# Performance work log

Hardware: AMD Instinct MI355X
Metric: run time of the kernel (lower is better)

The kernel has to match this reference:

```python
import jax, jax.numpy as jnp
import numpy as np

NUM_HEADS = 12

def _get_rel_pos(size, rel_pos):
    # q_size == k_size == size, no interpolation needed (table has 2*size-1 rows)
    idx = jnp.arange(size)[:, None] - jnp.arange(size)[None, :] + (size - 1)  # (size,size)
    return rel_pos[idx]  # (size, size, head_dim)

def setup_inputs() -> dict:
    key = jax.random.key(0)
    ks = jax.random.split(key, 7)
    B, H, W, dim = 8, 32, 32, 768
    head_dim = dim // NUM_HEADS
    return {
        "x": jax.random.normal(ks[0], (B, H, W, dim), jnp.float32),
        "qkv_w": jax.random.normal(ks[1], (dim, 3 * dim), jnp.float32) * 0.02,
        "qkv_b": jax.random.normal(ks[2], (3 * dim,), jnp.float32) * 0.02,
        "proj_w": jax.random.normal(ks[3], (dim, dim), jnp.float32) * 0.02,
        "proj_b": jax.random.normal(ks[4], (dim,), jnp.float32) * 0.02,
        "rel_pos_h": jax.random.normal(ks[5], (2 * H - 1, head_dim), jnp.float32) * 0.02,
        "rel_pos_w": jax.random.normal(ks[6], (2 * W - 1, head_dim), jnp.float32) * 0.02,
    }

def reference(x, qkv_w, qkv_b, proj_w, proj_b, rel_pos_h, rel_pos_w):
    B, H, W, dim = x.shape
    N = H * W
    head_dim = dim // NUM_HEADS
    scale = head_dim ** (-0.5)

    qkv = x.reshape(B, N, dim) @ qkv_w + qkv_b                     # (B,N,3*dim)
    qkv = qkv.reshape(B, N, 3, NUM_HEADS, head_dim)
    qkv = qkv.transpose(2, 0, 3, 1, 4).reshape(3, B * NUM_HEADS, N, head_dim)
    q, k, v = qkv[0], qkv[1], qkv[2]                               # (B*h, N, hd)

    attn = jnp.einsum("bnd,bmd->bnm", q * scale, k)                # (B*h, N, N)

    # decomposed relative position bias
    Rh = _get_rel_pos(H, rel_pos_h)                                # (H,H,hd)
    Rw = _get_rel_pos(W, rel_pos_w)                                # (W,W,hd)
    r_q = q.reshape(B * NUM_HEADS, H, W, head_dim)
    rel_h = jnp.einsum("bhwc,hkc->bhwk", r_q, Rh)                  # (B*h,H,W,H)
    rel_w = jnp.einsum("bhwc,wkc->bhwk", r_q, Rw)                  # (B*h,H,W,W)
    attn = (attn.reshape(B * NUM_HEADS, H, W, H, W)
            + rel_h[:, :, :, :, None]
            + rel_w[:, :, :, None, :]).reshape(B * NUM_HEADS, N, N)

    attn = jax.nn.softmax(attn, axis=-1)
    out = jnp.einsum("bnm,bmd->bnd", attn, v)                      # (B*h, N, hd)
    out = out.reshape(B, NUM_HEADS, H, W, head_dim).transpose(0, 2, 3, 1, 4).reshape(B, H, W, dim)
    return out @ proj_w + proj_b
```

## Files before the change

kernel.cpp:

```cpp
#include <hip/hip_runtime.h>
#include <hip/hip_bf16.h>
#include <math.h>

#define DIM   768
#define NHEAD 12
#define NQ    1024

typedef short  short8  __attribute__((ext_vector_type(8)));
typedef unsigned short us8 __attribute__((ext_vector_type(8)));
typedef float  f32x16  __attribute__((ext_vector_type(16)));

#if __has_builtin(__builtin_amdgcn_exp2f)
#define EXP2(x) __builtin_amdgcn_exp2f(x)
#else
#define EXP2(x) __expf(0.69314718056f * (x))
#endif
#define LOG2E 1.44269504089f

__device__ inline ushort f2b(float f) {
  union { float f; unsigned u; } c; c.f = f;
  unsigned r = (c.u + 0x7FFFu + ((c.u >> 16) & 1u)) >> 16;
  return (ushort)r;
}
__device__ inline float b2f(ushort h) {
  union { unsigned u; float f; } c; c.u = ((unsigned)h) << 16;
  return c.f;
}
__device__ inline ushort4 cvt4(float4 v) {
  ushort4 o; o.x = f2b(v.x); o.y = f2b(v.y); o.z = f2b(v.z); o.w = f2b(v.w);
  return o;
}
__device__ inline unsigned pkr(float a, float b) {
  union { float f; unsigned u; } ca, cb; ca.f = a; cb.f = b;
  return __builtin_amdgcn_perm(cb.u + 0x8000u, ca.u + 0x8000u, 0x07060302u);
}
__device__ __forceinline__ void gload16(const void* g, void* l) {
  __builtin_amdgcn_global_load_lds(
      (const __attribute__((address_space(1))) void*)g,
      (__attribute__((address_space(3))) void*)l, 16, 0, 0);
}

__global__ __launch_bounds__(256) void prep(
    const float* __restrict__ x, const float* __restrict__ qkv_w,
    const float* __restrict__ proj_w, ushort* __restrict__ Xb,
    ushort* __restrict__ Wqt, ushort* __restrict__ Wpt) {
  __shared__ ushort Ts[64][68];
  const int blk = blockIdx.x, tid = threadIdx.x;
  if (blk < 768) {
    const float4* src = (const float4*)x;
    ushort4* dst = (ushort4*)Xb;
    int base = blk * 2048;
#pragma unroll
    for (int it = 0; it < 8; ++it) {
      int i = base + it * 256 + tid;
      dst[i] = cvt4(src[i]);
    }
    return;
  }
  const float* W; ushort* Wt; int ncols, tk, tn;
  if (blk < 1200) { int t = blk - 768;  W = qkv_w; Wt = Wqt; ncols = 2304; tk = t % 12; tn = t / 12; }
  else            { int t = blk - 1200; W = proj_w; Wt = Wpt; ncols = 768; tk = t % 12; tn = t / 12; }
  const int kb = tk * 64, nb = tn * 64;
#pragma unroll
  for (int rr = 0; rr < 4; ++rr) {
    int r = (tid >> 4) + rr * 16, c4 = (tid & 15) * 4;
    float4 w = *(const float4*)(W + (size_t)(kb + r) * ncols + nb + c4);
    *(ushort4*)&Ts[r][c4] = cvt4(w);
  }
  __syncthreads();
#pragma unroll
  for (int wwi = 0; wwi < 2; ++wwi) {
    int n = (tid >> 3) + wwi * 32, k8 = (tid & 7) * 8;
    us8 v;
#pragma unroll
    for (int j = 0; j < 8; ++j) v[j] = Ts[k8 + j][n];
    *(us8*)(Wt + (size_t)(nb + n) * 768 + kb + k8) = v;
  }
}

__global__ __launch_bounds__(256, 4) void gemm_qkv(
    const ushort* __restrict__ A, const ushort* __restrict__ BT,
    const float* __restrict__ bias, ushort* __restrict__ Cp,
    ushort* __restrict__ VTg) {
  __shared__ __align__(16) ushort As[128 * 64];
  __shared__ __align__(16) ushort Bs[128 * 64];
  const int tid = threadIdx.x;
  const int flat = blockIdx.x;
  const int g = flat >> 3;
  const int by = (flat & 7) * 8 + g / 18;
  const int bx = g % 18;
  const int bm = by * 128, bn = bx * 128;
  const int lane = tid & 63, wv = tid >> 6;
  const int l31 = lane & 31, lh = lane >> 5;
  const int wm = (wv >> 1) * 64, wn = (wv & 1) * 64;
  const int xr = l31 & 7;

  const int dr = lane >> 3;
  const int ccol = ((lane & 7) ^ dr) * 8;
  const ushort* ag = A + (size_t)(bm + wv * 32 + dr) * 768 + ccol;
  const ushort* bg = BT + (size_t)(bn + wv * 32 + dr) * 768 + ccol;
  ushort* al = &As[wv * 32 * 64];
  ushort* bl = &Bs[wv * 32 * 64];

  f32x16 acc[2][2];
#pragma unroll
  for (int i = 0; i < 2; ++i)
#pragma unroll
    for (int j = 0; j < 2; ++j)
#pragma unroll
      for (int r = 0; r < 16; ++r) acc[i][j][r] = 0.f;

  for (int kt = 0; kt < 768; kt += 64) {
    __syncthreads();
#pragma unroll
    for (int wi = 0; wi < 4; ++wi) {
      gload16(ag + kt + wi * (8 * 768), al + wi * 512);
      gload16(bg + kt + wi * (8 * 768), bl + wi * 512);
    }
    __syncthreads();
#pragma unroll
    for (int ks = 0; ks < 4; ++ks) {
      const int ca = ((ks * 2 + lh) ^ xr) * 8;
      short8 a0 = *(const short8*)&As[(wm + l31) * 64 + ca];
      short8 a1 = *(const short8*)&As[(wm + 32 + l31) * 64 + ca];
      short8 b0 = *(const short8*)&Bs[(wn + l31) * 64 + ca];
      short8 b1 = *(const short8*)&Bs[(wn + 32 + l31) * 64 + ca];
      acc[0][0] = __builtin_amdgcn_mfma_f32_32x32x16_bf16(a0, b0, acc[0][0], 0, 0, 0);
      acc[0][1] = __builtin_amdgcn_mfma_f32_32x32x16_bf16(a0, b1, acc[0][1], 0, 0, 0);
      acc[1][0] = __builtin_amdgcn_mfma_f32_32x32x16_bf16(a1, b0, acc[1][0], 0, 0, 0);
      acc[1][1] = __builtin_amdgcn_mfma_f32_32x32x16_bf16(a1, b1, acc[1][1], 0, 0, 0);
    }
  }

  if (bn < 1536) {
#pragma unroll
    for (int mb = 0; mb < 2; ++mb)
#pragma unroll
      for (int nb = 0; nb < 2; ++nb) {
        int col = bn + wn + nb * 32 + l31;
        float bv = bias[col];
#pragma unroll
        for (int reg = 0; reg < 16; ++reg) {
          int row = bm + wm + mb * 32 + (reg & 3) + 8 * (reg >> 2) + 4 * lh;
          Cp[(size_t)row * 2304 + col] = f2b(acc[mb][nb][reg] + bv);
        }
      }
  } else {
    const int b_ = bm >> 10;
    const int nbase = (bm & 1023) + wm;
#pragma unroll
    for (int nb = 0; nb < 2; ++nb) {
      int col = bn + wn + nb * 32 + l31;
      float bv = bias[col];
      int hd_ = col - 1536;
      int h_ = hd_ >> 6, d_ = hd_ & 63;
      ushort* vrow = VTg + ((size_t)(b_ * NHEAD + h_) * 64 + d_) * NQ;
#pragma unroll
      for (int mb = 0; mb < 2; ++mb)
#pragma unroll
        for (int g2 = 0; g2 < 4; ++g2) {
          int n = nbase + mb * 32 + 8 * g2 + 4 * lh;
          ushort4 st;
          st.x = f2b(acc[mb][nb][4 * g2 + 0] + bv);
          st.y = f2b(acc[mb][nb][4 * g2 + 1] + bv);
          st.z = f2b(acc[mb][nb][4 * g2 + 2] + bv);
          st.w = f2b(acc[mb][nb][4 * g2 + 3] + bv);
          *(ushort4*)(vrow + n) = st;
        }
    }
  }
}

__global__ __launch_bounds__(256, 4) void gemm_proj(
    const ushort* __restrict__ A, const ushort* __restrict__ BT,
    const float* __restrict__ bias, float* __restrict__ C) {
  __shared__ __align__(16) ushort As[128 * 64];
  __shared__ __align__(16) ushort Bs[64 * 64];
  const int tid = threadIdx.x;
  const int flat = blockIdx.x;
  const int g = flat >> 3;
  const int by = (flat & 7) * 8 + g / 12;
  const int bx = g % 12;
  const int bm = by * 128, bn = bx * 64;
  const int lane = tid & 63, wv = tid >> 6;
  const int l31 = lane & 31, lh = lane >> 5;
  const int wm = (wv >> 1) * 64, wn = (wv & 1) * 32;
  const int xr = l31 & 7;

  const int dr = lane >> 3;
  const int ccol = ((lane & 7) ^ dr) * 8;
  const ushort* ag = A + (size_t)(bm + wv * 32 + dr) * 768 + ccol;
  const ushort* bg = BT + (size_t)(bn + wv * 16 + dr) * 768 + ccol;
  ushort* al = &As[wv * 32 * 64];
  ushort* bl = &Bs[wv * 16 * 64];

  f32x16 acc0, acc1;
#pragma unroll
  for (int r = 0; r < 16; ++r) { acc0[r] = 0.f; acc1[r] = 0.f; }

  for (int kt = 0; kt < 768; kt += 64) {
    __syncthreads();
#pragma unroll
    for (int wi = 0; wi < 4; ++wi)
      gload16(ag + kt + wi * (8 * 768), al + wi * 512);
    gload16(bg + kt,            bl);
    gload16(bg + kt + 8 * 768,  bl + 512);
    __syncthreads();
#pragma unroll
    for (int ks = 0; ks < 4; ++ks) {
      const int ca = ((ks * 2 + lh) ^ xr) * 8;
      short8 a0 = *(const short8*)&As[(wm + l31) * 64 + ca];
      short8 a1 = *(const short8*)&As[(wm + 32 + l31) * 64 + ca];
      short8 b0 = *(const short8*)&Bs[(wn + l31) * 64 + ca];
      acc0 = __builtin_amdgcn_mfma_f32_32x32x16_bf16(a0, b0, acc0, 0, 0, 0);
      acc1 = __builtin_amdgcn_mfma_f32_32x32x16_bf16(a1, b0, acc1, 0, 0, 0);
    }
  }

  const int col = bn + wn + l31;
  const float bv = bias[col];
#pragma unroll
  for (int reg = 0; reg < 16; ++reg) {
    int row = bm + wm + (reg & 3) + 8 * (reg >> 2) + 4 * lh;
    C[(size_t)row * 768 + col]        = acc0[reg] + bv;
    C[(size_t)(row + 32) * 768 + col] = acc1[reg] + bv;
  }
}

__global__ __launch_bounds__(256, 4) void attn_mfma(
    const ushort* __restrict__ QKV, const ushort* __restrict__ VTg,
    const float* __restrict__ rph, const float* __restrict__ rpw,
    ushort* __restrict__ O) {
  __shared__ ushort Qs[128][72];
  __shared__ __align__(16) ushort KV[2 * 64 * 64];

  ushort* const Ksp = KV;
  ushort* const VTp = KV + 64 * 64;

  const int tid = threadIdx.x;
  const int bh = blockIdx.x % 96;
  const int qt = blockIdx.x / 96;
  const int b = bh / NHEAD, h = bh % NHEAD;
  const int n0 = qt * 128;
  const int lane = tid & 63, wv = tid >> 6;
  const int l31 = lane & 31, lh = lane >> 5;
  const int wb = wv * 32;
  const int xr = l31 & 7;

  const ushort* qb = QKV + (size_t)b * NQ * 2304 + h * 64;
  const ushort* kb = qb + DIM;
  const ushort* vtg = VTg + (size_t)bh * 64 * NQ;

#pragma unroll
  for (int it = 0; it < 4; ++it) {
    int item = tid + 256 * it;
    int r = item >> 3, c8 = (item & 7) * 8;
    *(us8*)&Qs[r][c8] = *(const us8*)(qb + (size_t)(n0 + r) * 2304 + c8);
  }
#pragma unroll
  for (int it = 0; it < 4; ++it) {
    int item = tid + 256 * it;
    int r = item >> 4, c4 = (item & 15) * 4;
    if (r < 63) {
      float4 vh = *(const float4*)(rph + r * 64 + c4);
      vh.x *= LOG2E; vh.y *= LOG2E; vh.z *= LOG2E; vh.w *= LOG2E;
      *(ushort4*)&Ksp[r * 64 + c4] = cvt4(vh);
      float4 vw = *(const float4*)(rpw + r * 64 + c4);
      vw.x *= LOG2E; vw.y *= LOG2E; vw.z *= LOG2E; vw.w *= LOG2E;
      *(ushort4*)&VTp[r * 64 + c4] = cvt4(vw);
    } else {
      ushort4 z = {0, 0, 0, 0};
      *(ushort4*)&Ksp[r * 64 + c4] = z;
      *(ushort4*)&VTp[r * 64 + c4] = z;
    }
  }

  const int dr = lane >> 3;
  const int ccol = ((lane & 7) ^ dr) * 8;
  const ushort* kg = kb + (size_t)(wv * 16 + dr) * 2304 + ccol;
  const ushort* vg = vtg + (size_t)(wv * 16 + dr) * NQ + ccol;
  ushort* kl = &Ksp[wv * 16 * 64];
  ushort* vl = &VTp[wv * 16 * 64];

  __syncthreads();

  short8 aq[4];
#pragma unroll
  for (int ks = 0; ks < 4; ++ks)
    aq[ks] = *(const short8*)&Qs[wb + l31][ks * 16 + lh * 8];

  __syncthreads();

  ushort* Pb2 = &Qs[0][0] + wv * (32 * 40);
  ushort* rhs = &Qs[0][0] + 5120;

  {
    const int hq31 = qt * 4 + wv + 31;
    f32x16 sh;
#pragma unroll
    for (int i = 0; i < 16; ++i) sh[i] = 0.f;
#pragma unroll
    for (int ks = 0; ks < 4; ++ks) {
      short8 at = *(const short8*)&Ksp[(hq31 - l31) * 64 + ks * 16 + lh * 8];
      sh = __builtin_amdgcn_mfma_f32_32x32x16_bf16(at, aq[ks], sh, 0, 0, 0);
    }
#pragma unroll
    for (int reg = 0; reg < 16; ++reg) {
      int hk = (reg & 3) + 8 * (reg >> 2) + 4 * lh;
      rhs[hk * 128 + wb + l31] = f2b(sh[reg]);
    }
  }

  float rwv[16];
  {
    short8 at[8];
#pragma unroll
    for (int ub = 0; ub < 2; ++ub)
#pragma unroll
      for (int ks = 0; ks < 4; ++ks)
        at[ub * 4 + ks] =
            *(const short8*)&VTp[(ub * 32 + l31) * 64 + ks * 16 + lh * 8];
    f32x16 su0, su1;
#pragma unroll
    for (int i = 0; i < 16; ++i) { su0[i] = 0.f; su1[i] = 0.f; }
#pragma unroll
    for (int ks = 0; ks < 4; ++ks) {
      su0 = __builtin_amdgcn_mfma_f32_32x32x16_bf16(at[ks],     aq[ks], su0, 0, 0, 0);
      su1 = __builtin_amdgcn_mfma_f32_32x32x16_bf16(at[4 + ks], aq[ks], su1, 0, 0, 0);
    }
    __syncthreads();
#pragma unroll
    for (int reg = 0; reg < 16; ++reg) {
      int rm = (reg & 3) + 8 * (reg >> 2) + 4 * lh;
      KV[rm * 128 + wb + l31]        = f2b(su0[reg]);
      KV[(32 + rm) * 128 + wb + l31] = f2b(su1[reg]);
    }
#pragma unroll
    for (int reg = 0; reg < 16; ++reg) {
      int rm = (reg & 3) + 8 * (reg >> 2) + 4 * lh;
      rwv[reg] = b2f(KV[(31 + l31 - rm) * 128 + wb + l31]);
    }
  }

  f32x16 oacc0, oacc1;
#pragma unroll
  for (int i = 0; i < 16; ++i) { oacc0[i] = 0.f; oacc1[i] = 0.f; }
  float lacc = 0.f;

  for (int t = 0; t < 16; ++t) {
    const int kt = t * 64;
    __syncthreads();
    gload16(kg + (size_t)kt * 2304,              kl);
    gload16(kg + (size_t)kt * 2304 + 8 * 2304,   kl + 512);
    gload16(vg + kt,                             vl);
    gload16(vg + kt + 8 * NQ,                    vl + 512);
    __syncthreads();

    const float rh0 = b2f(rhs[(2 * t) * 128 + wb + l31]);
    const float rh1 = b2f(rhs[(2 * t + 1) * 128 + wb + l31]);

#pragma unroll
    for (int cb = 0; cb < 2; ++cb) {
      f32x16 s;
#pragma unroll
      for (int i = 0; i < 16; ++i) s[i] = 0.f;
#pragma unroll
      for (int ks = 0; ks < 4; ++ks) {
        const int ck = ((ks * 2 + lh) ^ xr) * 8;
        short8 ak = *(const short8*)&Ksp[(cb * 32 + l31) * 64 + ck];
        s = __builtin_amdgcn_mfma_f32_32x32x16_bf16(ak, aq[ks], s, 0, 0, 0);
      }
      const float rhv = cb ? rh1 : rh0;
#pragma unroll
      for (int g = 0; g < 4; ++g) {
        float p0 = EXP2(fmaf(s[4 * g + 0], 0.18033688f, rwv[4 * g + 0] + rhv));
        float p1 = EXP2(fmaf(s[4 * g + 1], 0.18033688f, rwv[4 * g + 1] + rhv));
        float p2 = EXP2(fmaf(s[4 * g + 2], 0.18033688f, rwv[4 * g + 2] + rhv));
        float p3 = EXP2(fmaf(s[4 * g + 3], 0.18033688f, rwv[4 * g + 3] + rhv));
        lacc += (p0 + p1) + (p2 + p3);
        uint2 pk; pk.x = pkr(p0, p1); pk.y = pkr(p2, p3);
        *(uint2*)&Pb2[l31 * 40 + 8 * g + 4 * lh] = pk;
      }
#pragma unroll
      for (int ks = 0; ks < 2; ++ks) {
        const int cv = ((cb * 4 + ks * 2 + lh) ^ xr) * 8;
        short8 ap  = *(const short8*)&Pb2[l31 * 40 + ks * 16 + lh * 8];
        short8 bv0 = *(const short8*)&VTp[l31 * 64 + cv];
        short8 bv1 = *(const short8*)&VTp[(32 + l31) * 64 + cv];
        oacc0 = __builtin_amdgcn_mfma_f32_32x32x16_bf16(ap, bv0, oacc0, 0, 0, 0);
        oacc1 = __builtin_amdgcn_mfma_f32_32x32x16_bf16(ap, bv1, oacc1, 0, 0, 0);
      }
    }
  }

  lacc += __shfl_xor(lacc, 32);
  const float linv = 1.0f / lacc;
  ushort* ob = O + ((size_t)b * NQ + n0 + wb) * DIM + h * 64;
#pragma unroll
  for (int reg = 0; reg < 16; ++reg) {
    int row = (reg & 3) + 8 * (reg >> 2) + 4 * lh;
    float lq = __shfl(linv, row);
    ob[(size_t)row * DIM + l31]      = f2b(oacc0[reg] * lq);
    ob[(size_t)row * DIM + 32 + l31] = f2b(oacc1[reg] * lq);
  }
}

extern "C" void kernel_launch(void* const* d_in, const int* in_sizes, int n_in,
                              void* d_out, int out_size, void* d_ws, size_t ws_size,
                              hipStream_t stream) {
  const float* x      = (const float*)d_in[0];
  const float* qkv_w  = (const float*)d_in[1];
  const float* qkv_b  = (const float*)d_in[2];
  const float* proj_w = (const float*)d_in[3];
  const float* proj_b = (const float*)d_in[4];
  const float* rel_h  = (const float*)d_in[5];
  const float* rel_w  = (const float*)d_in[6];
  float* out = (float*)d_out;

  ushort* qkvb = (ushort*)d_ws;
  ushort* obuf = qkvb + (size_t)8192 * 2304;
  ushort* Xb   = obuf + (size_t)8192 * DIM;
  ushort* Wqt  = Xb + (size_t)8192 * DIM;
  ushort* Wpt  = Wqt + (size_t)2304 * DIM;
  ushort* VTg  = Wpt + (size_t)DIM * DIM;

  prep<<<dim3(1344), 256, 0, stream>>>(x, qkv_w, proj_w, Xb, Wqt, Wpt);

  gemm_qkv<<<dim3(1152), 256, 0, stream>>>(Xb, Wqt, qkv_b, qkvb, VTg);

  attn_mfma<<<dim3(96 * 8), 256, 0, stream>>>(qkvb, VTg, rel_h, rel_w, obuf);

  gemm_proj<<<dim3(768), 256, 0, stream>>>(obuf, Wpt, proj_b, out);
}
```

Measured before the change: 192.6 us.

## Shrink attention LDS footprint to 32KB and raise occupancy to five blocks

Replaces the padded Q tile and separate K/V buffers with a single 32KB LDS array split into two regions, loads Q with direct global-to-LDS swizzled copies, and swizzles the rel-pos tables. The three rel-pos MFMA groups are now computed together after one barrier, and the P staging buffer drops its padding from 40 to 32 columns. The aim is to fit more blocks per CU (launch bounds 4 to 5) by cutting LDS and to remove a barrier in the prologue. The tighter register budget may cause spills, and the unpadded P buffer may see more bank conflicts.

```diff
diff --git a/kernel.cpp b/kernel.cpp
--- a/kernel.cpp
+++ b/kernel.cpp
@@ -227,15 +227,13 @@
   }
 }
 
-__global__ __launch_bounds__(256, 4) void attn_mfma(
+__global__ __launch_bounds__(256, 5) void attn_mfma(
     const ushort* __restrict__ QKV, const ushort* __restrict__ VTg,
     const float* __restrict__ rph, const float* __restrict__ rpw,
     ushort* __restrict__ O) {
-  __shared__ ushort Qs[128][72];
-  __shared__ __align__(16) ushort KV[2 * 64 * 64];
-
-  ushort* const Ksp = KV;
-  ushort* const VTp = KV + 64 * 64;
+  __shared__ __align__(16) ushort L[16384];
+  ushort* const R0 = L;
+  ushort* const R1 = L + 8192;
 
   const int tid = threadIdx.x;
   const int bh = blockIdx.x % 96;
@@ -251,96 +249,87 @@
   const ushort* kb = qb + DIM;
   const ushort* vtg = VTg + (size_t)bh * 64 * NQ;
 
-#pragma unroll
-  for (int it = 0; it < 4; ++it) {
-    int item = tid + 256 * it;
-    int r = item >> 3, c8 = (item & 7) * 8;
-    *(us8*)&Qs[r][c8] = *(const us8*)(qb + (size_t)(n0 + r) * 2304 + c8);
+  const int dr = lane >> 3;
+  const int ccol = ((lane & 7) ^ dr) * 8;
+
+  {
+    const ushort* qg = qb + (size_t)(n0 + wv * 32 + dr) * 2304 + ccol;
+    ushort* ql = R0 + wv * 32 * 64;
+#pragma unroll
+    for (int wi = 0; wi < 4; ++wi)
+      gload16(qg + (size_t)wi * 8 * 2304, ql + wi * 512);
   }
 #pragma unroll
   for (int it = 0; it < 4; ++it) {
     int item = tid + 256 * it;
     int r = item >> 4, c4 = (item & 15) * 4;
+    int sw = r * 64 + (((c4 >> 3) ^ (r & 7)) << 3) + (c4 & 7);
     if (r < 63) {
       float4 vh = *(const float4*)(rph + r * 64 + c4);
       vh.x *= LOG2E; vh.y *= LOG2E; vh.z *= LOG2E; vh.w *= LOG2E;
-      *(ushort4*)&Ksp[r * 64 + c4] = cvt4(vh);
+      *(ushort4*)&R1[sw] = cvt4(vh);
       float4 vw = *(const float4*)(rpw + r * 64 + c4);
       vw.x *= LOG2E; vw.y *= LOG2E; vw.z *= LOG2E; vw.w *= LOG2E;
-      *(ushort4*)&VTp[r * 64 + c4] = cvt4(vw);
+      *(ushort4*)&R1[4096 + sw] = cvt4(vw);
     } else {
       ushort4 z = {0, 0, 0, 0};
-      *(ushort4*)&Ksp[r * 64 + c4] = z;
-      *(ushort4*)&VTp[r * 64 + c4] = z;
-    }
-  }
-
-  const int dr = lane >> 3;
-  const int ccol = ((lane & 7) ^ dr) * 8;
+      *(ushort4*)&R1[sw] = z;
+      *(ushort4*)&R1[4096 + sw] = z;
+    }
+  }
+  __syncthreads();
+
+  short8 aq[4];
+#pragma unroll
+  for (int ks = 0; ks < 4; ++ks)
+    aq[ks] = *(const short8*)&R0[(wb + l31) * 64 + ((ks * 2 + lh) ^ xr) * 8];
+
+  const int rA = qt * 4 + wv + 31 - l31;
+  short8 ah[4];
+#pragma unroll
+  for (int ks = 0; ks < 4; ++ks)
+    ah[ks] = *(const short8*)&R1[rA * 64 + ((ks * 2 + lh) ^ (rA & 7)) * 8];
+  short8 aw[8];
+#pragma unroll
+  for (int ub = 0; ub < 2; ++ub) {
+    const int rB = ub * 32 + l31;
+#pragma unroll
+    for (int ks = 0; ks < 4; ++ks)
+      aw[ub * 4 + ks] =
+          *(const short8*)&R1[4096 + rB * 64 + ((ks * 2 + lh) ^ (rB & 7)) * 8];
+  }
+  __syncthreads();
+
+  f32x16 sh, su0, su1;
+#pragma unroll
+  for (int i = 0; i < 16; ++i) { sh[i] = 0.f; su0[i] = 0.f; su1[i] = 0.f; }
+#pragma unroll
+  for (int ks = 0; ks < 4; ++ks) {
+    sh  = __builtin_amdgcn_mfma_f32_32x32x16_bf16(ah[ks],     aq[ks], sh,  0, 0, 0);
+    su0 = __builtin_amdgcn_mfma_f32_32x32x16_bf16(aw[ks],     aq[ks], su0, 0, 0, 0);
+    su1 = __builtin_amdgcn_mfma_f32_32x32x16_bf16(aw[4 + ks], aq[ks], su1, 0, 0, 0);
+  }
+
+  ushort* Pb2 = R0 + wv * 1024;
+  ushort* rhs = R0 + 4096;
+#pragma unroll
+  for (int reg = 0; reg < 16; ++reg) {
+    int rm = (reg & 3) + 8 * (reg >> 2) + 4 * lh;
+    rhs[rm * 128 + wb + l31] = f2b(sh[reg]);
+    R1[rm * 128 + wb + l31]        = f2b(su0[reg]);
+    R1[(32 + rm) * 128 + wb + l31] = f2b(su1[reg]);
+  }
+  float rwv[16];
+#pragma unroll
+  for (int reg = 0; reg < 16; ++reg) {
+    int rm = (reg & 3) + 8 * (reg >> 2) + 4 * lh;
+    rwv[reg] = b2f(R1[(31 + l31 - rm) * 128 + wb + l31]);
+  }
+
   const ushort* kg = kb + (size_t)(wv * 16 + dr) * 2304 + ccol;
   const ushort* vg = vtg + (size_t)(wv * 16 + dr) * NQ + ccol;
-  ushort* kl = &Ksp[wv * 16 * 64];
-  ushort* vl = &VTp[wv * 16 * 64];
-
-  __syncthreads();
-
-  short8 aq[4];
-#pragma unroll
-  for (int ks = 0; ks < 4; ++ks)
-    aq[ks] = *(const short8*)&Qs[wb + l31][ks * 16 + lh * 8];
-
-  __syncthreads();
-
-  ushort* Pb2 = &Qs[0][0] + wv * (32 * 40);
-  ushort* rhs = &Qs[0][0] + 5120;
-
-  {
-    const int hq31 = qt * 4 + wv + 31;
-    f32x16 sh;
-#pragma unroll
-    for (int i = 0; i < 16; ++i) sh[i] = 0.f;
-#pragma unroll
-    for (int ks = 0; ks < 4; ++ks) {
-      short8 at = *(const short8*)&Ksp[(hq31 - l31) * 64 + ks * 16 + lh * 8];
-      sh = __builtin_amdgcn_mfma_f32_32x32x16_bf16(at, aq[ks], sh, 0, 0, 0);
-    }
-#pragma unroll
-    for (int reg = 0; reg < 16; ++reg) {
-      int hk = (reg & 3) + 8 * (reg >> 2) + 4 * lh;
-      rhs[hk * 128 + wb + l31] = f2b(sh[reg]);
-    }
-  }
-
-  float rwv[16];
-  {
-    short8 at[8];
-#pragma unroll
-    for (int ub = 0; ub < 2; ++ub)
-#pragma unroll
-      for (int ks = 0; ks < 4; ++ks)
-        at[ub * 4 + ks] =
-            *(const short8*)&VTp[(ub * 32 + l31) * 64 + ks * 16 + lh * 8];
-    f32x16 su0, su1;
-#pragma unroll
-    for (int i = 0; i < 16; ++i) { su0[i] = 0.f; su1[i] = 0.f; }
-#pragma unroll
-    for (int ks = 0; ks < 4; ++ks) {
-      su0 = __builtin_amdgcn_mfma_f32_32x32x16_bf16(at[ks],     aq[ks], su0, 0, 0, 0);
-      su1 = __builtin_amdgcn_mfma_f32_32x32x16_bf16(at[4 + ks], aq[ks], su1, 0, 0, 0);
-    }
-    __syncthreads();
-#pragma unroll
-    for (int reg = 0; reg < 16; ++reg) {
-      int rm = (reg & 3) + 8 * (reg >> 2) + 4 * lh;
-      KV[rm * 128 + wb + l31]        = f2b(su0[reg]);
-      KV[(32 + rm) * 128 + wb + l31] = f2b(su1[reg]);
-    }
-#pragma unroll
-    for (int reg = 0; reg < 16; ++reg) {
-      int rm = (reg & 3) + 8 * (reg >> 2) + 4 * lh;
-      rwv[reg] = b2f(KV[(31 + l31 - rm) * 128 + wb + l31]);
-    }
-  }
+  ushort* kl = R1 + wv * 16 * 64;
+  ushort* vl = R1 + 4096 + wv * 16 * 64;
 
   f32x16 oacc0, oacc1;
 #pragma unroll
@@ -367,7 +356,7 @@
 #pragma unroll
       for (int ks = 0; ks < 4; ++ks) {
         const int ck = ((ks * 2 + lh) ^ xr) * 8;
-        short8 ak = *(const short8*)&Ksp[(cb * 32 + l31) * 64 + ck];
+        short8 ak = *(const short8*)&R1[(cb * 32 + l31) * 64 + ck];
         s = __builtin_amdgcn_mfma_f32_32x32x16_bf16(ak, aq[ks], s, 0, 0, 0);
       }
       const float rhv = cb ? rh1 : rh0;
@@ -379,14 +368,14 @@
         float p3 = EXP2(fmaf(s[4 * g + 3], 0.18033688f, rwv[4 * g + 3] + rhv));
         lacc += (p0 + p1) + (p2 + p3);
         uint2 pk; pk.x = pkr(p0, p1); pk.y = pkr(p2, p3);
-        *(uint2*)&Pb2[l31 * 40 + 8 * g + 4 * lh] = pk;
+        *(uint2*)&Pb2[l31 * 32 + 8 * g + 4 * lh] = pk;
       }
 #pragma unroll
       for (int ks = 0; ks < 2; ++ks) {
         const int cv = ((cb * 4 + ks * 2 + lh) ^ xr) * 8;
-        short8 ap  = *(const short8*)&Pb2[l31 * 40 + ks * 16 + lh * 8];
-        short8 bv0 = *(const short8*)&VTp[l31 * 64 + cv];
-        short8 bv1 = *(const short8*)&VTp[(32 + l31) * 64 + cv];
+        short8 ap  = *(const short8*)&Pb2[l31 * 32 + ks * 16 + lh * 8];
+        short8 bv0 = *(const short8*)&R1[4096 + l31 * 64 + cv];
+        short8 bv1 = *(const short8*)&R1[4096 + (32 + l31) * 64 + cv];
         oacc0 = __builtin_amdgcn_mfma_f32_32x32x16_bf16(ap, bv0, oacc0, 0, 0, 0);
         oacc1 = __builtin_amdgcn_mfma_f32_32x32x16_bf16(ap, bv1, oacc1, 0, 0, 0);
       }
```

After: 239.3 us. +24.2%, slower.
